# Kernel tuning notes

Measured on AMD Instinct MI355X. Metric: run time of the kernel, lower is better.

Reference implementation:

```python
import jax, jax.numpy as jnp
import numpy as np

STRIDE = 1
PAD = 1

def setup_inputs() -> dict:
    key = jax.random.key(0)
    k1, k2 = jax.random.split(key)
    x = jax.random.normal(k1, (32, 128, 56, 56), dtype=jnp.float32)
    W = jax.random.normal(k2, (256, 128, 3, 3), dtype=jnp.float32)
    b = jnp.zeros((256,), dtype=jnp.float32)
    return {"x": x, "W": W, "b": b}

def reference(x, W, b):
    # Faithful conv2d: NCHW input, OIHW weight, stride 1, pad 1, plus bias.
    out = jax.lax.conv_general_dilated(
        x, W,
        window_strides=(STRIDE, STRIDE),
        padding=((PAD, PAD), (PAD, PAD)),
        dimension_numbers=("NCHW", "OIHW", "NCHW"),
    )
    return out + b[None, :, None, None]
```

## Files before the change

kernel.cpp:

```cpp
#include <hip/hip_runtime.h>
#include <hip/hip_bf16.h>
#include <cstdint>
#include <cstddef>

#define NB   32
#define CIN  128
#define HWP  3136
#define KOC  256
#define NRS  9
#define PROW 3364
#define GUARD 256
#define AEL  12288
#define BEL  8192

typedef __attribute__((ext_vector_type(8))) short  short8;
typedef __attribute__((ext_vector_type(4))) short  short4v;
typedef __attribute__((ext_vector_type(4))) float  float4v;

__device__ __forceinline__ unsigned short f2bf(float f) {
    union { float f; unsigned int u; } v; v.f = f;
    unsigned int u = v.u;
    u = u + 0x7fffu + ((u >> 16) & 1u);
    return (unsigned short)(u >> 16);
}

__global__ __launch_bounds__(256) void prep_kernel(const float* __restrict__ W,
                                                   unsigned short* __restrict__ wt2,
                                                   const float* __restrict__ x,
                                                   unsigned short* __restrict__ xt) {
    __shared__ unsigned short lds[32 * 260];
    int blk = blockIdx.x;
    int t   = threadIdx.x;

    if (blk < 1152) {
        int idx  = blk * 256 + t;
        int e    = idx & 7;
        int lr   = (idx >> 3) & 15;
        int quad = (idx >> 7) & 3;
        int i    = (idx >> 9) & 3;
        int wm   = (idx >> 11) & 1;
        int rem  = idx >> 12;
        int s    = rem % 3;
        int q    = rem / 3;
        int ot   = q & 1;
        int r    = (q >> 1) % 3;
        int ck   = q / 6;
        int oc = ot * 128 + wm * 64 + i * 16 + lr;
        int c  = ck * 32 + quad * 8 + e;
        wt2[idx] = f2bf(W[((size_t)oc * CIN + c) * NRS + r * 3 + s]);
        return;
    }

    if (blk >= 2816) {
        int g = (blk - 2816) * 256 + t;
        int slab = g / 228;
        int gi   = g - slab * 228;
        int row;
        if (gi < 59)       row = gi;
        else if (gi < 169) { int k = gi - 59;
                             row = 115 + 58 * (k >> 1) + (k & 1); }
        else               row = 3305 + (gi - 169);
        unsigned short* gr = xt + (size_t)slab * (PROW * 32) + (size_t)row * 32;
        short8 z = (short8)0;
        *(short8*)(gr +  0) = z;
        *(short8*)(gr +  8) = z;
        *(short8*)(gr + 16) = z;
        *(short8*)(gr + 24) = z;
        return;
    }

    int b    = blk - 1152;
    int tile = b % 13;
    int ck   = (b / 13) & 3;
    int n    = b / 52;
    int hw0  = tile * 256;
    int wv   = t >> 6;
    int lane = t & 63;

    const float* src = x + ((size_t)(n * CIN + ck * 32)) * HWP;
    #pragma unroll
    for (int pass = 0; pass < 8; ++pass) {
        int c  = pass * 4 + wv;
        int hw = hw0 + lane * 4;
        if (hw < HWP) {
            float4v v = *(const float4v*)(src + (size_t)c * HWP + hw);
            short4v s4;
            #pragma unroll
            for (int k = 0; k < 4; ++k) s4[k] = (short)f2bf(v[k]);
            *(short4v*)(&lds[c * 260 + lane * 4]) = s4;
        }
    }
    __syncthreads();

    int sub = t & 3;
    int hwl = t >> 2;
    unsigned short* dst = xt + ((size_t)(n * 4 + ck)) * PROW * 32;
    #pragma unroll
    for (int pass = 0; pass < 4; ++pass) {
        int hl = pass * 64 + hwl;
        int hw = hw0 + hl;
        if (hw < HWP) {
            short8 v;
            #pragma unroll
            for (int j = 0; j < 8; ++j)
                v[j] = (short)lds[(sub * 8 + j) * 260 + hl];
            int pr = hw + 59 + 2 * (hw / 56);
            *(short8*)(dst + (size_t)pr * 32 + sub * 8) = v;
        }
    }
}

__device__ __forceinline__ void stage_A(const unsigned short* src,
                                        unsigned short* lbase,
                                        int wv, int lane) {
    #pragma unroll
    for (int it = 0; it < 6; ++it) {
        int c0 = it * 256 + wv * 64;
        __builtin_amdgcn_global_load_lds(
            (const __attribute__((address_space(1))) void*)(src + (size_t)(c0 + lane) * 8),
            (__attribute__((address_space(3))) void*)(lbase + (size_t)c0 * 8), 16, 0, 0);
    }
}

__device__ __forceinline__ void stage_B(const unsigned short* gwin,
                                        unsigned short* lbase,
                                        int wv, int lane) {
    #pragma unroll
    for (int it = 0; it < 4; ++it) {
        int blk = it * 4 + wv;
        int s   = blk * 64 + lane;
        int r   = s >> 2;
        int q   = s & 3;
        int qs  = q ^ ((r >> 1) & 3);
        __builtin_amdgcn_global_load_lds(
            (const __attribute__((address_space(1))) void*)(gwin + r * 32 + qs * 8),
            (__attribute__((address_space(3))) void*)(lbase + (size_t)blk * 512), 16, 0, 0);
    }
}

__device__ __forceinline__ short8 ldb(const char* lb, int r, int quad) {
    int q = quad ^ ((r >> 1) & 3);
    return *(const short8*)(lb + r * 64 + q * 16);
}

__global__ __launch_bounds__(256, 3) void gemm_kernel(const unsigned short* __restrict__ xt,
                                                      const unsigned short* __restrict__ wt2,
                                                      const float* __restrict__ bias,
                                                      float* __restrict__ out) {
    __shared__ unsigned short lds[20480];

    int bx0 = blockIdx.x;
    int bx  = (bx0 & 7) * 200 + (bx0 >> 3);
    int ot  = bx & 1;
    int n   = (bx >> 1) & 31;
    int pt  = bx >> 6;
    int p0  = pt * 128;

    int t    = threadIdx.x;
    int wv   = t >> 6;
    int lane = t & 63;
    int lr   = lane & 15;
    int quad = lane >> 4;
    int wm   = wv >> 1;
    int wn   = wv & 1;

    int prbase = p0 + 2 * (p0 / 56);

    int rb[4];
    #pragma unroll
    for (int j = 0; j < 4; ++j) {
        int hw  = p0 + wn * 64 + j * 16 + lr;
        int hwc = hw < HWP ? hw : (HWP - 1);
        rb[j] = hwc + 59 + 2 * (hwc / 56) - prbase;
    }

    const unsigned short* xb = xt + (size_t)n * 4 * PROW * 32;
    const unsigned short* wb = wt2 + ot * AEL;

    float4v acc[4][4];
    #pragma unroll
    for (int i = 0; i < 4; ++i)
        #pragma unroll
        for (int j = 0; j < 4; ++j)
            acc[i][j] = (float4v){0.f, 0.f, 0.f, 0.f};

    for (int ck = 0; ck < 4; ++ck) {
        for (int r = 0; r < 3; ++r) {
            stage_A(wb + (size_t)ck * 73728 + (size_t)r * 24576, lds, wv, lane);
            if (r == 0)
                stage_B(xb + (size_t)ck * (PROW * 32) + (size_t)prbase * 32,
                        lds + 12288, wv, lane);
            __syncthreads();

            const unsigned short* A = lds + wm * 2048 + lane * 8;
            const char* lbB = (const char*)(lds + 12288);
            int sh0 = (r - 1) * 58;

            #pragma unroll
            for (int s = 0; s < 3; ++s) {
                int shift = sh0 + s - 1;
                short8 af[4];
                #pragma unroll
                for (int i = 0; i < 4; ++i)
                    af[i] = *(const short8*)(A + s * 4096 + i * 512);
                short8 bcur = ldb(lbB, rb[0] + shift, quad);
                __builtin_amdgcn_s_setprio(1);
                #pragma unroll
                for (int j = 0; j < 4; ++j) {
                    short8 bnext;
                    if (j < 3) bnext = ldb(lbB, rb[j + 1] + shift, quad);
                    #pragma unroll
                    for (int i = 0; i < 4; ++i)
                        acc[i][j] = __builtin_amdgcn_mfma_f32_16x16x32_bf16(
                            af[i], bcur, acc[i][j], 0, 0, 0);
                    if (j < 3) bcur = bnext;
                }
                __builtin_amdgcn_s_setprio(0);
            }
            __syncthreads();
        }
    }

    float* orow = out + (size_t)n * KOC * HWP;
    #pragma unroll
    for (int i = 0; i < 4; ++i) {
        #pragma unroll
        for (int rr = 0; rr < 4; ++rr) {
            int oc = ot * 128 + wm * 64 + i * 16 + quad * 4 + rr;
            float bi = bias[oc];
            #pragma unroll
            for (int j = 0; j < 4; ++j) {
                int hw = p0 + wn * 64 + j * 16 + lr;
                if (hw < HWP)
                    orow[(size_t)oc * HWP + hw] = acc[i][j][rr] + bi;
            }
        }
    }
}

__global__ void naive_kernel(const float* __restrict__ x, const float* __restrict__ W,
                             const float* __restrict__ b, float* __restrict__ out) {
    size_t idx = (size_t)blockIdx.x * 256 + threadIdx.x;
    if (idx >= (size_t)NB * KOC * HWP) return;
    int w0 = (int)(idx % 56);
    int h0 = (int)((idx / 56) % 56);
    int k  = (int)((idx / HWP) % KOC);
    int n  = (int)(idx / ((size_t)HWP * KOC));
    float acc = b[k];
    for (int c = 0; c < CIN; ++c) {
        const float* xr = x + ((size_t)n * CIN + c) * HWP;
        const float* wr = W + ((size_t)k * CIN + c) * NRS;
        for (int r = 0; r < 3; ++r) {
            int h = h0 + r - 1;
            if ((unsigned)h >= 56u) continue;
            for (int s = 0; s < 3; ++s) {
                int w = w0 + s - 1;
                if ((unsigned)w >= 56u) continue;
                acc += xr[h * 56 + w] * wr[r * 3 + s];
            }
        }
    }
    out[idx] = acc;
}

extern "C" void kernel_launch(void* const* d_in, const int* in_sizes, int n_in,
                              void* d_out, int out_size, void* d_ws, size_t ws_size,
                              hipStream_t stream) {
    const float* x  = (const float*)d_in[0];
    const float* W  = (const float*)d_in[1];
    const float* b  = (const float*)d_in[2];
    float* out = (float*)d_out;

    const size_t wt_elems = (size_t)NRS * 4 * 2 * 2 * 4 * 4 * 16 * 8;
    const size_t xt_elems = (size_t)NB * 4 * PROW * 32 + (size_t)GUARD * 32;
    const size_t need = (wt_elems + xt_elems) * sizeof(unsigned short);

    if (ws_size < need) {
        size_t total = (size_t)NB * KOC * HWP;
        naive_kernel<<<(unsigned)((total + 255) / 256), 256, 0, stream>>>(x, W, b, out);
        return;
    }

    unsigned short* wt2 = (unsigned short*)d_ws;
    unsigned short* xt  = wt2 + wt_elems;

    prep_kernel<<<1152 + NB * 4 * 13 + 114, 256, 0, stream>>>(W, wt2, x, xt);
    gemm_kernel<<<1600, 256, 0, stream>>>(xt, wt2, b, out);
}
```

Baseline: 209.1 us.

## Pipeline weight taps through a 4-slot LDS ring with vmcnt waits

Reorders the prepped weight layout so each of the 36 (ck,r,s) taps is a contiguous 4096-element tile per output-channel half. The GEMM loop now streams one tap at a time into a 4-slot LDS ring, prefetching three taps ahead. It synchronises with explicit s_waitcnt vmcnt plus s_barrier instead of reloading a whole row of taps between two __syncthreads. This overlaps global-to-LDS weight loads with MFMA work. In exchange it uses more LDS (48KB, which may reduce occupancy), and the input slab reload between channel chunks stays serialized.

```diff
diff --git a/kernel.cpp b/kernel.cpp
--- a/kernel.cpp
+++ b/kernel.cpp
@@ -10,12 +10,14 @@
 #define NRS  9
 #define PROW 3364
 #define GUARD 256
-#define AEL  12288
+#define TEL  4096
 #define BEL  8192
 
 typedef __attribute__((ext_vector_type(8))) short  short8;
 typedef __attribute__((ext_vector_type(4))) short  short4v;
 typedef __attribute__((ext_vector_type(4))) float  float4v;
+
+#define VM_WAIT(n) asm volatile("s_waitcnt vmcnt(" #n ")" ::: "memory")
 
 __device__ __forceinline__ unsigned short f2bf(float f) {
     union { float f; unsigned int u; } v; v.f = f;
@@ -39,12 +41,12 @@
         int quad = (idx >> 7) & 3;
         int i    = (idx >> 9) & 3;
         int wm   = (idx >> 11) & 1;
-        int rem  = idx >> 12;
-        int s    = rem % 3;
-        int q    = rem / 3;
-        int ot   = q & 1;
-        int r    = (q >> 1) % 3;
-        int ck   = q / 6;
+        int q    = idx >> 12;
+        int tap  = q % 36;
+        int ot   = q / 36;
+        int s    = tap % 3;
+        int r    = (tap / 3) % 3;
+        int ck   = tap / 9;
         int oc = ot * 128 + wm * 64 + i * 16 + lr;
         int c  = ck * 32 + quad * 8 + e;
         wt2[idx] = f2bf(W[((size_t)oc * CIN + c) * NRS + r * 3 + s]);
@@ -110,15 +112,15 @@
     }
 }
 
-__device__ __forceinline__ void stage_A(const unsigned short* src,
-                                        unsigned short* lbase,
-                                        int wv, int lane) {
-    #pragma unroll
-    for (int it = 0; it < 6; ++it) {
+__device__ __forceinline__ void stage_A_tap(const unsigned short* src,
+                                            unsigned short* dstbuf,
+                                            int wv, int lane) {
+    #pragma unroll
+    for (int it = 0; it < 2; ++it) {
         int c0 = it * 256 + wv * 64;
         __builtin_amdgcn_global_load_lds(
             (const __attribute__((address_space(1))) void*)(src + (size_t)(c0 + lane) * 8),
-            (__attribute__((address_space(3))) void*)(lbase + (size_t)c0 * 8), 16, 0, 0);
+            (__attribute__((address_space(3))) void*)(dstbuf + (size_t)c0 * 8), 16, 0, 0);
     }
 }
 
@@ -147,7 +149,7 @@
                                                       const unsigned short* __restrict__ wt2,
                                                       const float* __restrict__ bias,
                                                       float* __restrict__ out) {
-    __shared__ unsigned short lds[20480];
+    __shared__ unsigned short lds[24576];
 
     int bx0 = blockIdx.x;
     int bx  = (bx0 & 7) * 200 + (bx0 >> 3);
@@ -175,7 +177,7 @@
     }
 
     const unsigned short* xb = xt + (size_t)n * 4 * PROW * 32;
-    const unsigned short* wb = wt2 + ot * AEL;
+    const unsigned short* wa = wt2 + (size_t)ot * 147456;
 
     float4v acc[4][4];
     #pragma unroll
@@ -184,40 +186,54 @@
         for (int j = 0; j < 4; ++j)
             acc[i][j] = (float4v){0.f, 0.f, 0.f, 0.f};
 
+    stage_B(xb + (size_t)prbase * 32, lds + 16384, wv, lane);
+    stage_A_tap(wa,            lds,            wv, lane);
+    stage_A_tap(wa + TEL,      lds + TEL,      wv, lane);
+    stage_A_tap(wa + 2 * TEL,  lds + 2 * TEL,  wv, lane);
+
+    const char* lbB = (const char*)(lds + 16384);
+
+    #pragma unroll
     for (int ck = 0; ck < 4; ++ck) {
-        for (int r = 0; r < 3; ++r) {
-            stage_A(wb + (size_t)ck * 73728 + (size_t)r * 24576, lds, wv, lane);
-            if (r == 0)
-                stage_B(xb + (size_t)ck * (PROW * 32) + (size_t)prbase * 32,
-                        lds + 12288, wv, lane);
-            __syncthreads();
-
-            const unsigned short* A = lds + wm * 2048 + lane * 8;
-            const char* lbB = (const char*)(lds + 12288);
-            int sh0 = (r - 1) * 58;
-
-            #pragma unroll
-            for (int s = 0; s < 3; ++s) {
-                int shift = sh0 + s - 1;
-                short8 af[4];
+        #pragma unroll
+        for (int tc = 0; tc < 9; ++tc) {
+            const int tp = ck * 9 + tc;
+            if ((tc == 0 && ck > 0) || tp == 35) VM_WAIT(0);
+            else if (tp == 34)                   VM_WAIT(2);
+            else                                 VM_WAIT(4);
+            __builtin_amdgcn_s_barrier();
+            __builtin_amdgcn_sched_barrier(0);
+
+            if (tp <= 32)
+                stage_A_tap(wa + (size_t)(tp + 3) * TEL,
+                            lds + ((tp + 3) & 3) * TEL, wv, lane);
+
+            const unsigned short* A = lds + (tp & 3) * TEL + wm * 2048 + lane * 8;
+            const int shift = (tc / 3 - 1) * 58 + (tc % 3) - 1;
+
+            short8 af[4];
+            #pragma unroll
+            for (int i = 0; i < 4; ++i)
+                af[i] = *(const short8*)(A + i * 512);
+            short8 bcur = ldb(lbB, rb[0] + shift, quad);
+            __builtin_amdgcn_s_setprio(1);
+            #pragma unroll
+            for (int j = 0; j < 4; ++j) {
+                short8 bnext;
+                if (j < 3) bnext = ldb(lbB, rb[j + 1] + shift, quad);
                 #pragma unroll
                 for (int i = 0; i < 4; ++i)
-                    af[i] = *(const short8*)(A + s * 4096 + i * 512);
-                short8 bcur = ldb(lbB, rb[0] + shift, quad);
-                __builtin_amdgcn_s_setprio(1);
-                #pragma unroll
-                for (int j = 0; j < 4; ++j) {
-                    short8 bnext;
-                    if (j < 3) bnext = ldb(lbB, rb[j + 1] + shift, quad);
-                    #pragma unroll
-                    for (int i = 0; i < 4; ++i)
-                        acc[i][j] = __builtin_amdgcn_mfma_f32_16x16x32_bf16(
-                            af[i], bcur, acc[i][j], 0, 0, 0);
-                    if (j < 3) bcur = bnext;
-                }
-                __builtin_amdgcn_s_setprio(0);
+                    acc[i][j] = __builtin_amdgcn_mfma_f32_16x16x32_bf16(
+                        af[i], bcur, acc[i][j], 0, 0, 0);
+                if (j < 3) bcur = bnext;
             }
-            __syncthreads();
+            __builtin_amdgcn_s_setprio(0);
+
+            if (tc == 8 && ck < 3) {
+                __builtin_amdgcn_s_barrier();
+                stage_B(xb + (size_t)(ck + 1) * (PROW * 32) + (size_t)prbase * 32,
+                        lds + 16384, wv, lane);
+            }
         }
     }
 
```

Result: faster. 202.7 us (-3.1%).
